# Optimization experiments

Measured on AMD Instinct MI355X. Metric: run time of the kernel, lower is better.

## Reference

```python
import jax, jax.numpy as jnp
import numpy as np

BLOCK = 8
ITERS = 8
EPS = 1e-5
SHAPE = (64, 64, 64)
BATCH = 16


def overlapping_blocks(x, bs):
    # x: [B, M, N, K] -> per-block copies with a 1-cell zero-padded halo:
    # [B, nm, nn, nk, bs+2, bs+2, bs+2]
    B, M, N, K = x.shape
    p = jnp.pad(x, ((0, 0), (1, 1), (1, 1), (1, 1)))

    def gather(a, axis, n, size):
        idx = (jnp.arange(n)[:, None] * bs + jnp.arange(size)[None, :]).reshape(-1)
        a = jnp.take(a, idx, axis=axis)
        return a.reshape(a.shape[:axis] + (n, size) + a.shape[axis + 1:])

    nm, nn, nk = M // bs, N // bs, K // bs
    p = gather(p, 1, nm, bs + 2)   # [B, nm, P, N+2, K+2]
    p = gather(p, 3, nn, bs + 2)   # [B, nm, P, nn, P, K+2]
    p = gather(p, 5, nk, bs + 2)   # [B, nm, P, nn, P, nk, P]
    return p.transpose(0, 1, 3, 5, 2, 4, 6)


def param_blocks(w, bs):
    # [..., M, N, K] -> [..., nm, nn, nk, bs, bs, bs] (non-overlapping)
    lead = w.shape[:-3]
    M, N, K = w.shape[-3:]
    w = w.reshape(*lead, M // bs, bs, N // bs, bs, K // bs, bs)
    nl = len(lead)
    perm = tuple(range(nl)) + (nl, nl + 2, nl + 4, nl + 1, nl + 3, nl + 5)
    return w.transpose(perm)


def gridnet_step(weight, bias, residual_scale, x, inner_iterations, block_size,
                 eps=EPS, normalize=True):
    bs = block_size
    blocks = overlapping_blocks(x, bs)            # [B, nm, nn, nk, P, P, P]
    wb = param_blocks(weight, bs)                 # [27, nm, nn, nk, bs, bs, bs]
    bb = param_blocks(bias, bs)                   # [nm, nn, nk, bs, bs, bs]
    rb = param_blocks(residual_scale, bs)
    inner = (slice(None),) * 4 + (slice(1, -1),) * 3

    for _ in range(inner_iterations):
        if normalize:
            mean = blocks.mean(axis=(-3, -2, -1), keepdims=True)
            var = blocks.var(axis=(-3, -2, -1), keepdims=True)
            normed = (blocks - mean) / jnp.sqrt(var + eps)
        else:
            normed = blocks
        dot = jnp.zeros_like(blocks[inner])
        tap = 0
        for dx in range(3):
            for dy in range(3):
                for dz in range(3):
                    nb = normed[..., dx:dx + bs, dy:dy + bs, dz:dz + bs]
                    dot = dot + nb * wb[tap]
                    tap += 1
        out = blocks[inner] + rb * jax.nn.silu(dot + bb)
        # only interior cells update; halo stays at initial (synced) values
        blocks = blocks.at[inner].set(out)

    y = blocks[inner]                              # [B, nm, nn, nk, bs, bs, bs]
    B, nm, nn, nk = y.shape[:4]
    return y.transpose(0, 1, 4, 2, 5, 3, 6).reshape(B, nm * bs, nn * bs, nk * bs)


def setup_inputs() -> dict:
    key = jax.random.key(0)
    k_w, k_x = jax.random.split(key)
    M, N, K = SHAPE
    weight = jax.random.normal(k_w, (27, M, N, K), dtype=jnp.float32) / np.sqrt(27.0).astype(np.float32)
    bias = jnp.zeros((M, N, K), dtype=jnp.float32)
    residual_scale = jnp.ones((M, N, K), dtype=jnp.float32)
    x = jax.random.normal(k_x, (BATCH, M, N, K), dtype=jnp.float32)
    return {"weight": weight, "bias": bias, "residual_scale": residual_scale, "x": x}


def reference(weight, bias, residual_scale, x):
    return gridnet_step(weight, bias, residual_scale, x, ITERS, BLOCK, EPS, True)
```

## Files before the change

### kernel.cpp

```cpp
#include <hip/hip_runtime.h>

typedef _Float16 h2 __attribute__((ext_vector_type(2)));

#define CSTR 7
#define COLH 14

template <int CTRL>
__device__ __forceinline__ float dpp_stage(float v) {
    int x = __builtin_amdgcn_update_dpp(0, __float_as_int(v), CTRL, 0xf, 0xf, true);
    return v + __int_as_float(x);
}
__device__ __forceinline__ float wave_sum(float v) {
    v = dpp_stage<0x111>(v);
    v = dpp_stage<0x112>(v);
    v = dpp_stage<0x114>(v);
    v = dpp_stage<0x118>(v);
    v = dpp_stage<0x142>(v);
    v = dpp_stage<0x143>(v);
    return v;
}

#define RFL(x) __int_as_float(__builtin_amdgcn_readfirstlane(__float_as_int(x)))

__device__ __forceinline__ h2 mid2(h2 lo, h2 hi) {
    int r = __builtin_amdgcn_alignbit(__builtin_bit_cast(int, hi),
                                      __builtin_bit_cast(int, lo), 16);
    return __builtin_bit_cast(h2, r);
}
__device__ __forceinline__ h2 pkrtz(float a, float b) {
    return __builtin_bit_cast(h2, __builtin_amdgcn_cvt_pkrtz(a, b));
}

#define R27(M) M(0) M(1) M(2) M(3) M(4) M(5) M(6) M(7) M(8) M(9) M(10) M(11) \
    M(12) M(13) M(14) M(15) M(16) M(17) M(18) M(19) M(20) M(21) M(22) M(23)  \
    M(24) M(25) M(26)

#define LOADW(T)                                                               \
    float4 f##T = *(const float4*)(W + ((size_t)(T) << 18) + ofs);             \
    h2 w##T##p = pkrtz(f##T.x, f##T.y);                                        \
    h2 w##T##q = pkrtz(f##T.z, f##T.w);                                        \
    sw0 += f##T.x; sw1 += f##T.y; sw2 += f##T.z; sw3 += f##T.w;

#define COLN(BP, O, T0, T1, T2, D0N, D1N) {                                    \
    h2 d0 = BP[(O)], d1 = BP[(O) + 1], d2 = BP[(O) + 2];                       \
    h2 m0 = mid2(d0, d1), m1 = mid2(d1, d2);                                   \
    D0N = __builtin_elementwise_fma(d0, w##T0##p, D0N);                        \
    D1N = __builtin_elementwise_fma(d1, w##T0##q, D1N);                        \
    D0N = __builtin_elementwise_fma(m0, w##T1##p, D0N);                        \
    D1N = __builtin_elementwise_fma(m1, w##T1##q, D1N);                        \
    D0N = __builtin_elementwise_fma(d1, w##T2##p, D0N);                        \
    D1N = __builtin_elementwise_fma(d2, w##T2##q, D1N); }

#define DOT27(BP, D0N, D1N)                                                    \
    COLN(BP, 0,    0,  1,  2, D0N, D1N)                                        \
    COLN(BP, 7,    3,  4,  5, D0N, D1N)                                        \
    COLN(BP, 14,   6,  7,  8, D0N, D1N)                                        \
    COLN(BP, 70,   9, 10, 11, D0N, D1N)                                        \
    COLN(BP, 77,  12, 13, 14, D0N, D1N)                                        \
    COLN(BP, 84,  15, 16, 17, D0N, D1N)                                        \
    COLN(BP, 140, 18, 19, 20, D0N, D1N)                                        \
    COLN(BP, 147, 21, 22, 23, D0N, D1N)                                        \
    COLN(BP, 154, 24, 25, 26, D0N, D1N)

#define SILU(U) ((U) * __builtin_amdgcn_rcpf(1.f + __expf(-(U))))

#define EPI4(DD0, DD1, SI, QI, HS, HQ, C0, C1, C2, C3, DSTB) {                 \
    float mean = (HS + SI) * inv_n;                                            \
    float istd = rsqrtf((HQ + QI) * inv_n - mean * mean + 1e-5f);              \
    float u0 = ((float)DD0.x - mean * sw0) * istd + bf.x;                      \
    float u1 = ((float)DD0.y - mean * sw1) * istd + bf.y;                      \
    float u2 = ((float)DD1.x - mean * sw2) * istd + bf.z;                      \
    float u3 = ((float)DD1.y - mean * sw3) * istd + bf.w;                      \
    C0 += rf.x * SILU(u0);                                                     \
    C1 += rf.y * SILU(u1);                                                     \
    C2 += rf.z * SILU(u2);                                                     \
    C3 += rf.w * SILU(u3);                                                     \
    DSTB[ipc] = (_Float16)C0;                                                  \
    *(h2*)&DSTB[ipc + 1] = pkrtz(C1, C2);                                      \
    DSTB[ipc + 3] = (_Float16)C3;  }

#define ITERP(BPA, DSTA, BPB, DSTB, RED) {                                     \
    h2 ddA0 = { (_Float16)0.f, (_Float16)0.f };                                \
    h2 ddA1 = ddA0, ddB0 = ddA0, ddB1 = ddA0;                                  \
    DOT27(BPA, ddA0, ddA1)                                                     \
    DOT27(BPB, ddB0, ddB1)                                                     \
    EPI4(ddA0, ddA1, SiA, QiA, halo_sA, halo_qA, cA0, cA1, cA2, cA3, DSTA)     \
    EPI4(ddB0, ddB1, SiB, QiB, halo_sB, halo_qB, cB0, cB1, cB2, cB3, DSTB)     \
    float spA = wave_sum((cA0 + cA1) + (cA2 + cA3));                           \
    float qpA = wave_sum((cA0 * cA0 + cA1 * cA1) + (cA2 * cA2 + cA3 * cA3));   \
    float spB = wave_sum((cB0 + cB1) + (cB2 + cB3));                           \
    float qpB = wave_sum((cB0 * cB0 + cB1 * cB1) + (cB2 * cB2 + cB3 * cB3));   \
    if (lane == 63) { RED[pg][0][wv1] = make_float2(spA, qpA);                 \
                      RED[pg][1][wv1] = make_float2(spB, qpB); }               \
    __syncthreads();                                                           \
    SiA = RFL(RED[pg][0][0].x + RED[pg][0][1].x);                              \
    QiA = RFL(RED[pg][0][0].y + RED[pg][0][1].y);                              \
    SiB = RFL(RED[pg][1][0].x + RED[pg][1][1].x);                              \
    QiB = RFL(RED[pg][1][0].y + RED[pg][1][1].y); }

__global__ __launch_bounds__(256)
void gridnet_kernel(const float* __restrict__ W,
                    const float* __restrict__ Bias,
                    const float* __restrict__ Rs,
                    const float* __restrict__ X,
                    float* __restrict__ Y,
                    int n_batch)
{
    __shared__ __align__(16) _Float16 buf[4][2][100 * COLH];
    __shared__ float4 red4[4][4];
    __shared__ float2 redP[2][2][2][2];

    const int tid = threadIdx.x;
    const int h    = tid & 1;
    const int ly   = (tid >> 1) & 7;
    const int lx   = (tid >> 4) & 7;
    const int pg   = tid >> 7;
    const int wave = tid >> 6;
    const int lane = tid & 63;
    const int wv1  = wave & 1;

    const int np    = n_batch >> 2;
    const int bid   = blockIdx.x;
    const int r     = bid / np;
    const int qb    = bid - r * np;
    const int batch0 = 4 * qb;
    const int gm0 = (r >> 6) << 3;
    const int gn0 = ((r >> 3) & 7) << 3;
    const int gk0 = (r & 7) << 3;

    const float* xb = X + ((size_t)batch0 << 18);

    float sA_all = 0.f, qA_all = 0.f, sA_int = 0.f, qA_int = 0.f;
    float sB_all = 0.f, qB_all = 0.f, sB_int = 0.f, qB_int = 0.f;
    float sC_all = 0.f, qC_all = 0.f, sC_int = 0.f, qC_int = 0.f;
    float sD_all = 0.f, qD_all = 0.f, sD_int = 0.f, qD_int = 0.f;
    for (int i = tid; i < 1000; i += 256) {
        int ix = i / 100;
        int rem = i - ix * 100;
        int iy = rem / 10;
        int iz = rem - iy * 10;
        int m = gm0 + ix - 1, n = gn0 + iy - 1, k = gk0 + iz - 1;
        float vA = 0.f, vB = 0.f, vC = 0.f, vD = 0.f;
        if ((unsigned)m < 64u && (unsigned)n < 64u && (unsigned)k < 64u) {
            const float* p = xb + (m << 12) + (n << 6) + k;
            vA = p[0];
            vB = p[1 << 18];
            vC = p[2 << 18];
            vD = p[3 << 18];
        }
        _Float16 hA = (_Float16)vA, hB = (_Float16)vB;
        _Float16 hC = (_Float16)vC, hD = (_Float16)vD;
        int a = (ix * 10 + iy) * COLH + iz;
        buf[0][0][a] = hA; buf[0][1][a] = hA;
        buf[1][0][a] = hB; buf[1][1][a] = hB;
        buf[2][0][a] = hC; buf[2][1][a] = hC;
        buf[3][0][a] = hD; buf[3][1][a] = hD;
        float fA = (float)hA, fB = (float)hB, fC = (float)hC, fD = (float)hD;
        sA_all += fA; qA_all += fA * fA;
        sB_all += fB; qB_all += fB * fB;
        sC_all += fC; qC_all += fC * fC;
        sD_all += fD; qD_all += fD * fD;
        bool interior = ((unsigned)(ix - 1) < 8u) & ((unsigned)(iy - 1) < 8u) &
                        ((unsigned)(iz - 1) < 8u);
        if (interior) { sA_int += fA; qA_int += fA * fA;
                        sB_int += fB; qB_int += fB * fB;
                        sC_int += fC; qC_int += fC * fC;
                        sD_int += fD; qD_int += fD * fD; }
    }

    {
        float a0 = wave_sum(sA_all), a1 = wave_sum(qA_all);
        float a2 = wave_sum(sA_int), a3 = wave_sum(qA_int);
        float b0 = wave_sum(sB_all), b1 = wave_sum(qB_all);
        float b2 = wave_sum(sB_int), b3 = wave_sum(qB_int);
        float c0 = wave_sum(sC_all), c1 = wave_sum(qC_all);
        float c2 = wave_sum(sC_int), c3 = wave_sum(qC_int);
        float d0 = wave_sum(sD_all), d1 = wave_sum(qD_all);
        float d2 = wave_sum(sD_int), d3 = wave_sum(qD_int);
        if (lane == 63) {
            red4[0][wave] = make_float4(a0, a1, a2, a3);
            red4[1][wave] = make_float4(b0, b1, b2, b3);
            red4[2][wave] = make_float4(c0, c1, c2, c3);
            red4[3][wave] = make_float4(d0, d1, d2, d3);
        }
    }

    const int gm = gm0 + lx, gn = gn0 + ly;
    const size_t ofs = ((size_t)gm << 12) + (gn << 6) + gk0 + 4 * h;
    float sw0 = 0.f, sw1 = 0.f, sw2 = 0.f, sw3 = 0.f;
    R27(LOADW)
    const float4 bf = *(const float4*)(Bias + ofs);
    const float4 rf = *(const float4*)(Rs + ofs);

    __syncthreads();

    float SA = 0.f, QA = 0.f, SiA = 0.f, QiA = 0.f;
    float SB = 0.f, QB = 0.f, SiB = 0.f, QiB = 0.f;
    #pragma unroll
    for (int wv = 0; wv < 4; ++wv) {
        float4 tA = red4[2 * pg][wv];
        float4 tB = red4[2 * pg + 1][wv];
        SA += tA.x; QA += tA.y; SiA += tA.z; QiA += tA.w;
        SB += tB.x; QB += tB.y; SiB += tB.z; QiB += tB.w;
    }
    const float halo_sA = RFL(SA - SiA), halo_qA = RFL(QA - QiA);
    const float halo_sB = RFL(SB - SiB), halo_qB = RFL(QB - QiB);
    SiA = RFL(SiA); QiA = RFL(QiA);
    SiB = RFL(SiB); QiB = RFL(QiB);

    const int bpD = (lx * 10 + ly) * CSTR + 2 * h;
    const h2* const bpA0 = (const h2*)buf[2 * pg][0] + bpD;
    const h2* const bpA1 = (const h2*)buf[2 * pg][1] + bpD;
    const h2* const bpB0 = (const h2*)buf[2 * pg + 1][0] + bpD;
    const h2* const bpB1 = (const h2*)buf[2 * pg + 1][1] + bpD;
    _Float16* const wrA0 = buf[2 * pg][0];
    _Float16* const wrA1 = buf[2 * pg][1];
    _Float16* const wrB0 = buf[2 * pg + 1][0];
    _Float16* const wrB1 = buf[2 * pg + 1][1];
    const int ipc = ((lx + 1) * 10 + (ly + 1)) * COLH + 4 * h + 1;
    float cA0 = (float)wrA0[ipc],     cA1 = (float)wrA0[ipc + 1];
    float cA2 = (float)wrA0[ipc + 2], cA3 = (float)wrA0[ipc + 3];
    float cB0 = (float)wrB0[ipc],     cB1 = (float)wrB0[ipc + 1];
    float cB2 = (float)wrB0[ipc + 2], cB3 = (float)wrB0[ipc + 3];

    const float inv_n = 1.0f / 1000.0f;

    #pragma unroll 1
    for (int it = 0; it < 4; ++it) {
        ITERP(bpA0, wrA1, bpB0, wrB1, redP[0])
        ITERP(bpA1, wrA0, bpB1, wrB0, redP[1])
    }

    float* yp = Y + ((size_t)(batch0 + 2 * pg) << 18) + ofs;
    *(float4*)yp = make_float4(cA0, cA1, cA2, cA3);
    *(float4*)(yp + (1 << 18)) = make_float4(cB0, cB1, cB2, cB3);
}

extern "C" void kernel_launch(void* const* d_in, const int* in_sizes, int n_in,
                              void* d_out, int out_size, void* d_ws, size_t ws_size,
                              hipStream_t stream) {
    const float* W = (const float*)d_in[0];
    const float* B = (const float*)d_in[1];
    const float* R = (const float*)d_in[2];
    const float* X = (const float*)d_in[3];
    float* Y = (float*)d_out;

    int n_batch = in_sizes[3] >> 18;
    dim3 grid(512 * (n_batch >> 2)), block(256);
    hipLaunchKernelGGL(gridnet_kernel, grid, block, 0, stream, W, B, R, X, Y, n_batch);
}
```

Measured before the change: 155.1 us.

## Shrink workgroups to 128 threads handling two batches each

Each workgroup now processes two batch elements with two waves instead of four batch elements with four waves, which doubles the grid size. The per-iteration __syncthreads then spans only two waves and shared memory per block is halved, which should improve occupancy and scheduling flexibility. The cost is that the weight, bias and residual loads for each spatial block are repeated across twice as many workgroups.

```diff
diff --git a/kernel.cpp b/kernel.cpp
--- a/kernel.cpp
+++ b/kernel.cpp
@@ -90,15 +90,15 @@
     float qpA = wave_sum((cA0 * cA0 + cA1 * cA1) + (cA2 * cA2 + cA3 * cA3));   \
     float spB = wave_sum((cB0 + cB1) + (cB2 + cB3));                           \
     float qpB = wave_sum((cB0 * cB0 + cB1 * cB1) + (cB2 * cB2 + cB3 * cB3));   \
-    if (lane == 63) { RED[pg][0][wv1] = make_float2(spA, qpA);                 \
-                      RED[pg][1][wv1] = make_float2(spB, qpB); }               \
+    if (lane == 63) { RED[0][wave] = make_float2(spA, qpA);                    \
+                      RED[1][wave] = make_float2(spB, qpB); }                  \
     __syncthreads();                                                           \
-    SiA = RFL(RED[pg][0][0].x + RED[pg][0][1].x);                              \
-    QiA = RFL(RED[pg][0][0].y + RED[pg][0][1].y);                              \
-    SiB = RFL(RED[pg][1][0].x + RED[pg][1][1].x);                              \
-    QiB = RFL(RED[pg][1][0].y + RED[pg][1][1].y); }
-
-__global__ __launch_bounds__(256)
+    SiA = RFL(RED[0][0].x + RED[0][1].x);                                      \
+    QiA = RFL(RED[0][0].y + RED[0][1].y);                                      \
+    SiB = RFL(RED[1][0].x + RED[1][1].x);                                      \
+    QiB = RFL(RED[1][0].y + RED[1][1].y); }
+
+__global__ __launch_bounds__(128)
 void gridnet_kernel(const float* __restrict__ W,
                     const float* __restrict__ Bias,
                     const float* __restrict__ Rs,
@@ -106,24 +106,22 @@
                     float* __restrict__ Y,
                     int n_batch)
 {
-    __shared__ __align__(16) _Float16 buf[4][2][100 * COLH];
-    __shared__ float4 red4[4][4];
-    __shared__ float2 redP[2][2][2][2];
+    __shared__ __align__(16) _Float16 buf[2][2][100 * COLH];
+    __shared__ float4 red4[2][2];
+    __shared__ float2 redP[2][2][2];
 
     const int tid = threadIdx.x;
     const int h    = tid & 1;
     const int ly   = (tid >> 1) & 7;
     const int lx   = (tid >> 4) & 7;
-    const int pg   = tid >> 7;
     const int wave = tid >> 6;
     const int lane = tid & 63;
-    const int wv1  = wave & 1;
-
-    const int np    = n_batch >> 2;
+
+    const int np    = n_batch >> 1;
     const int bid   = blockIdx.x;
     const int r     = bid / np;
-    const int qb    = bid - r * np;
-    const int batch0 = 4 * qb;
+    const int pb    = bid - r * np;
+    const int batch0 = 2 * pb;
     const int gm0 = (r >> 6) << 3;
     const int gn0 = ((r >> 3) & 7) << 3;
     const int gk0 = (r & 7) << 3;
@@ -132,40 +130,29 @@
 
     float sA_all = 0.f, qA_all = 0.f, sA_int = 0.f, qA_int = 0.f;
     float sB_all = 0.f, qB_all = 0.f, sB_int = 0.f, qB_int = 0.f;
-    float sC_all = 0.f, qC_all = 0.f, sC_int = 0.f, qC_int = 0.f;
-    float sD_all = 0.f, qD_all = 0.f, sD_int = 0.f, qD_int = 0.f;
-    for (int i = tid; i < 1000; i += 256) {
+    for (int i = tid; i < 1000; i += 128) {
         int ix = i / 100;
         int rem = i - ix * 100;
         int iy = rem / 10;
         int iz = rem - iy * 10;
         int m = gm0 + ix - 1, n = gn0 + iy - 1, k = gk0 + iz - 1;
-        float vA = 0.f, vB = 0.f, vC = 0.f, vD = 0.f;
+        float vA = 0.f, vB = 0.f;
         if ((unsigned)m < 64u && (unsigned)n < 64u && (unsigned)k < 64u) {
             const float* p = xb + (m << 12) + (n << 6) + k;
             vA = p[0];
             vB = p[1 << 18];
-            vC = p[2 << 18];
-            vD = p[3 << 18];
         }
         _Float16 hA = (_Float16)vA, hB = (_Float16)vB;
-        _Float16 hC = (_Float16)vC, hD = (_Float16)vD;
         int a = (ix * 10 + iy) * COLH + iz;
         buf[0][0][a] = hA; buf[0][1][a] = hA;
         buf[1][0][a] = hB; buf[1][1][a] = hB;
-        buf[2][0][a] = hC; buf[2][1][a] = hC;
-        buf[3][0][a] = hD; buf[3][1][a] = hD;
-        float fA = (float)hA, fB = (float)hB, fC = (float)hC, fD = (float)hD;
+        float fA = (float)hA, fB = (float)hB;
         sA_all += fA; qA_all += fA * fA;
         sB_all += fB; qB_all += fB * fB;
-        sC_all += fC; qC_all += fC * fC;
-        sD_all += fD; qD_all += fD * fD;
         bool interior = ((unsigned)(ix - 1) < 8u) & ((unsigned)(iy - 1) < 8u) &
                         ((unsigned)(iz - 1) < 8u);
         if (interior) { sA_int += fA; qA_int += fA * fA;
-                        sB_int += fB; qB_int += fB * fB;
-                        sC_int += fC; qC_int += fC * fC;
-                        sD_int += fD; qD_int += fD * fD; }
+                        sB_int += fB; qB_int += fB * fB; }
     }
 
     {
@@ -173,15 +160,9 @@
         float a2 = wave_sum(sA_int), a3 = wave_sum(qA_int);
         float b0 = wave_sum(sB_all), b1 = wave_sum(qB_all);
         float b2 = wave_sum(sB_int), b3 = wave_sum(qB_int);
-        float c0 = wave_sum(sC_all), c1 = wave_sum(qC_all);
-        float c2 = wave_sum(sC_int), c3 = wave_sum(qC_int);
-        float d0 = wave_sum(sD_all), d1 = wave_sum(qD_all);
-        float d2 = wave_sum(sD_int), d3 = wave_sum(qD_int);
         if (lane == 63) {
             red4[0][wave] = make_float4(a0, a1, a2, a3);
             red4[1][wave] = make_float4(b0, b1, b2, b3);
-            red4[2][wave] = make_float4(c0, c1, c2, c3);
-            red4[3][wave] = make_float4(d0, d1, d2, d3);
         }
     }
 
@@ -197,9 +178,9 @@
     float SA = 0.f, QA = 0.f, SiA = 0.f, QiA = 0.f;
     float SB = 0.f, QB = 0.f, SiB = 0.f, QiB = 0.f;
     #pragma unroll
-    for (int wv = 0; wv < 4; ++wv) {
-        float4 tA = red4[2 * pg][wv];
-        float4 tB = red4[2 * pg + 1][wv];
+    for (int wv = 0; wv < 2; ++wv) {
+        float4 tA = red4[0][wv];
+        float4 tB = red4[1][wv];
         SA += tA.x; QA += tA.y; SiA += tA.z; QiA += tA.w;
         SB += tB.x; QB += tB.y; SiB += tB.z; QiB += tB.w;
     }
@@ -209,14 +190,14 @@
     SiB = RFL(SiB); QiB = RFL(QiB);
 
     const int bpD = (lx * 10 + ly) * CSTR + 2 * h;
-    const h2* const bpA0 = (const h2*)buf[2 * pg][0] + bpD;
-    const h2* const bpA1 = (const h2*)buf[2 * pg][1] + bpD;
-    const h2* const bpB0 = (const h2*)buf[2 * pg + 1][0] + bpD;
-    const h2* const bpB1 = (const h2*)buf[2 * pg + 1][1] + bpD;
-    _Float16* const wrA0 = buf[2 * pg][0];
-    _Float16* const wrA1 = buf[2 * pg][1];
-    _Float16* const wrB0 = buf[2 * pg + 1][0];
-    _Float16* const wrB1 = buf[2 * pg + 1][1];
+    const h2* const bpA0 = (const h2*)buf[0][0] + bpD;
+    const h2* const bpA1 = (const h2*)buf[0][1] + bpD;
+    const h2* const bpB0 = (const h2*)buf[1][0] + bpD;
+    const h2* const bpB1 = (const h2*)buf[1][1] + bpD;
+    _Float16* const wrA0 = buf[0][0];
+    _Float16* const wrA1 = buf[0][1];
+    _Float16* const wrB0 = buf[1][0];
+    _Float16* const wrB1 = buf[1][1];
     const int ipc = ((lx + 1) * 10 + (ly + 1)) * COLH + 4 * h + 1;
     float cA0 = (float)wrA0[ipc],     cA1 = (float)wrA0[ipc + 1];
     float cA2 = (float)wrA0[ipc + 2], cA3 = (float)wrA0[ipc + 3];
@@ -231,7 +212,7 @@
         ITERP(bpA1, wrA0, bpB1, wrB0, redP[1])
     }
 
-    float* yp = Y + ((size_t)(batch0 + 2 * pg) << 18) + ofs;
+    float* yp = Y + ((size_t)batch0 << 18) + ofs;
     *(float4*)yp = make_float4(cA0, cA1, cA2, cA3);
     *(float4*)(yp + (1 << 18)) = make_float4(cB0, cB1, cB2, cB3);
 }
@@ -246,6 +227,6 @@
     float* Y = (float*)d_out;
 
     int n_batch = in_sizes[3] >> 18;
-    dim3 grid(512 * (n_batch >> 2)), block(256);
+    dim3 grid(512 * (n_batch >> 1)), block(128);
     hipLaunchKernelGGL(gridnet_kernel, grid, block, 0, stream, W, B, R, X, Y, n_batch);
 }
```

Result: no change. 153.3 us (-1.2%).
